# Performance work log

Hardware: AMD Instinct MI355X
Metric: run time of the kernel (lower is better)

## Reference

```python
import jax, jax.numpy as jnp
import numpy as np

B, LC, LE, H, V = 128, 256, 257, 512, 128
PAD = 0  # padding_token_index


def lstm_cell(x, h, c, Wih, Whh, b):
    # torch LSTMCell gate order: i, f, g, o
    g = x @ Wih.T + h @ Whh.T + b
    i, f, gg, o = jnp.split(g, 4, axis=-1)
    c = jax.nn.sigmoid(f) * c + jax.nn.sigmoid(i) * jnp.tanh(gg)
    h = jax.nn.sigmoid(o) * jnp.tanh(c)
    return h, c


def setup_inputs() -> dict:
    key = jax.random.key(0)
    ks = jax.random.split(key, 32)
    p = lambda k, shape: jax.random.normal(k, shape, jnp.float32) * 0.05
    d = {
        'C_idx': jax.random.randint(ks[0], (B, LC), 0, V, dtype=jnp.int32),
        'E_idx': jax.random.randint(ks[1], (B, LE), 0, V, dtype=jnp.int32),
        'C_pad': jnp.zeros((B, LC), dtype=bool),
        'enc_Wih_f': p(ks[2], (4 * H, V)),
        'enc_Whh_f': p(ks[3], (4 * H, H)),
        'enc_b_f': p(ks[4], (4 * H,)),
        'enc_Wih_b': p(ks[5], (4 * H, V)),
        'enc_Whh_b': p(ks[6], (4 * H, H)),
        'enc_b_b': p(ks[7], (4 * H,)),
        'dec_Wih': p(ks[8], (4 * H, H + V)),
        'dec_Whh': p(ks[9], (4 * H, H)),
        'dec_b': p(ks[10], (4 * H,)),
        'Wh': p(ks[11], (H, 2 * H)),
        'Wc': p(ks[12], (H, 2 * H)),
        'Wattn': p(ks[13], (H, 2 * H)),
        'Wout': p(ks[14], (H, 3 * H)),
        'Wvocab': p(ks[15], (V, H)),
        'pg_ctx': p(ks[16], (2 * H,)),
        'pg_in': p(ks[17], (V + H,)),
        'pg_h': p(ks[18], (H,)),
        'pg_c': p(ks[19], (H,)),
        'pg_b': p(ks[20], (1,)),
    }
    return d


def _forward(C_idx, E_idx, C_pad, enc_Wih_f, enc_Whh_f, enc_b_f, enc_Wih_b, enc_Whh_b, enc_b_b,
             dec_Wih, dec_Whh, dec_b, Wh, Wc, Wattn, Wout, Wvocab,
             pg_ctx, pg_in, pg_h, pg_c, pg_b):
    C = jax.nn.one_hot(C_idx, V, dtype=jnp.float32)      # [B,LC,V]
    E_emb = jax.nn.one_hot(E_idx, V, dtype=jnp.float32)  # [B,LE,V]
    z = jnp.zeros((B, H), jnp.float32)

    xs = jnp.swapaxes(C, 0, 1)  # [LC,B,V]

    def enc_fwd(carry, x):
        h, c = lstm_cell(x, carry[0], carry[1], enc_Wih_f, enc_Whh_f, enc_b_f)
        return (h, c), h

    def enc_bwd(carry, x):
        h, c = lstm_cell(x, carry[0], carry[1], enc_Wih_b, enc_Whh_b, enc_b_b)
        return (h, c), h

    (hf, cf), Hf = jax.lax.scan(enc_fwd, (z, z), xs)
    (hb, cb), Hb = jax.lax.scan(enc_bwd, (z, z), xs[::-1])
    Hb = Hb[::-1]
    enc = jnp.swapaxes(jnp.concatenate([Hf, Hb], axis=-1), 0, 1)  # [B,LC,2H]

    # decoder init state from final encoder states (fwd;bwd concat)
    h0 = jnp.concatenate([hf, hb], axis=-1) @ Wh.T
    c0 = jnp.concatenate([cf, cb], axis=-1) @ Wc.T

    enc_proj = enc @ Wattn.T  # [B,LC,H]

    def step(carry, x_emb):
        h, c, prev_out = carry
        nin = jnp.concatenate([x_emb, prev_out], axis=1)  # [B,V+H]
        h, c = lstm_cell(nin, h, c, dec_Wih, dec_Whh, dec_b)
        scores = jnp.einsum('blh,bh->bl', enc_proj, h)
        scores = jnp.where(C_pad, -jnp.inf, scores)
        attn = jax.nn.softmax(scores, axis=1)             # [B,LC]
        ctx = jnp.einsum('bl,blh->bh', attn, enc)         # [B,2H]
        t_out = jnp.tanh(jnp.concatenate([h, ctx], axis=1) @ Wout.T)  # [B,H]
        gen = jax.nn.softmax(t_out @ Wvocab.T, axis=1)    # [B,V]
        p_gen = jax.nn.sigmoid(ctx @ pg_ctx + nin @ pg_in + h @ pg_h + c @ pg_c + pg_b[0])[:, None]
        copy_p = attn * (1.0 - p_gen)
        out = jax.vmap(lambda o, idx, a: o.at[idx].add(a))(gen * p_gen, C_idx, copy_p)
        return (h, c, t_out), out

    xs2 = jnp.swapaxes(E_emb[:, :LE - 1], 0, 1)  # teacher inputs, step 0 = start token
    _, preds = jax.lax.scan(step, (h0, c0, z), xs2)
    preds = jnp.swapaxes(preds, 0, 1)  # [B,LE-1,V]

    tgt = E_idx[:, 1:]
    nll = -jnp.take_along_axis(jnp.log(preds), tgt[..., None], axis=2)[..., 0]
    return jnp.where(tgt == PAD, 0.0, nll)  # [B,LE-1], reduction='none'


def reference(C_idx, E_idx, C_pad, enc_Wih_f, enc_Whh_f, enc_b_f, enc_Wih_b, enc_Whh_b, enc_b_b,
              dec_Wih, dec_Whh, dec_b, Wh, Wc, Wattn, Wout, Wvocab,
              pg_ctx, pg_in, pg_h, pg_c, pg_b):
    return _forward(C_idx, E_idx, C_pad, enc_Wih_f, enc_Whh_f, enc_b_f, enc_Wih_b, enc_Whh_b, enc_b_b,
                    dec_Wih, dec_Whh, dec_b, Wh, Wc, Wattn, Wout, Wvocab,
                    pg_ctx, pg_in, pg_h, pg_c, pg_b)
```

## Files before the change

kernel.cpp:

```cpp
#include <hip/hip_runtime.h>

static constexpr size_t OFF_ENC   = 0;
static constexpr size_t OFF_WGE   = 67108864;
static constexpr size_t OFF_WIHTE = 71303168;
static constexpr size_t OFF_HENC  = 72351744;
static constexpr size_t OFF_CENC  = 72876032;
static constexpr size_t OFF_WGATE = 67108864;
static constexpr size_t OFF_XDEC  = 71303168;
static constexpr size_t OFF_WATTT = 71827456;
static constexpr size_t OFF_WOUT  = 72876032;
static constexpr size_t OFF_WVOCT = 74448896;
static constexpr size_t OFF_HDEC  = 74579968;
static constexpr size_t OFF_CDEC  = 74842112;
static constexpr size_t OFF_TOUT  = 75104256;
static constexpr size_t OFF_UFB   = 75366400;
static constexpr size_t OFF_CTXF  = 75628544;
static constexpr size_t OFF_CTXP  = 75890688;
static constexpr size_t OFF_SC    = 76414976;
static constexpr size_t OFF_MSP   = 76480512;
static constexpr size_t OFF_MD    = 76482560;

__device__ __forceinline__ float sigm(float x) { return 1.f / (1.f + expf(-x)); }
__device__ __forceinline__ unsigned short f2bf(float f) {
  unsigned u = __float_as_uint(f);
  u += 0x7fffu + ((u >> 16) & 1u);
  return (unsigned short)(u >> 16);
}
__device__ __forceinline__ float bfl(unsigned w) { return __uint_as_float(w << 16); }
__device__ __forceinline__ float bfh(unsigned w) { return __uint_as_float(w & 0xffff0000u); }
__device__ __forceinline__ float bf2f(unsigned short v) { return __uint_as_float(((unsigned)v) << 16); }

#if defined(__has_builtin)
#if __has_builtin(__builtin_amdgcn_fdot2_f32_bf16)
#define HAVE_DOT2BF 1
#endif
#endif
#ifdef HAVE_DOT2BF
typedef __bf16 bf2_t __attribute__((ext_vector_type(2)));
__device__ __forceinline__ float dot2bf(unsigned w, unsigned h, float acc) {
  return __builtin_amdgcn_fdot2_f32_bf16(__builtin_bit_cast(bf2_t, w),
                                         __builtin_bit_cast(bf2_t, h), acc, false);
}
#else
__device__ __forceinline__ float dot2bf(unsigned w, unsigned h, float acc) {
  return acc + bfl(w) * bfl(h) + bfh(w) * bfh(h);
}
#endif

__global__ __launch_bounds__(256) void k_pre1(const float* __restrict__ WhhF,
                                              const float* __restrict__ WhhB,
                                              const float* __restrict__ WihF,
                                              const float* __restrict__ WihB,
                                              char* __restrict__ wsb) {
  unsigned short* WGE = (unsigned short*)(wsb + OFF_WGE);
  unsigned short* WIH = (unsigned short*)(wsb + OFF_WIHTE);
  int id = blockIdx.x * 256 + threadIdx.x, str = gridDim.x * 256;
  for (int x = id; x < 2 * 2048 * 512; x += str) {
    int dir = x >> 20, r = (x >> 9) & 2047, k = x & 511;
    const float* W = dir ? WhhB : WhhF;
    WGE[x] = f2bf(W[(size_t)r * 512 + k]);
  }
  for (int x = id; x < 2 * 128 * 2048; x += str) {
    int dir = x >> 18, v = (x >> 11) & 127, r = x & 2047;
    const float* W = dir ? WihB : WihF;
    WIH[x] = f2bf(W[(size_t)r * 128 + v]);
  }
}

__global__ __launch_bounds__(256) void k_pre2(const float* __restrict__ dWih,
                                              const float* __restrict__ dWhh,
                                              const float* __restrict__ Wattn,
                                              const float* __restrict__ Wout,
                                              const float* __restrict__ Wvoc,
                                              char* __restrict__ wsb) {
  unsigned short* WG = (unsigned short*)(wsb + OFF_WGATE);
  unsigned short* XD = (unsigned short*)(wsb + OFF_XDEC);
  unsigned short* WA = (unsigned short*)(wsb + OFF_WATTT);
  unsigned short* WO = (unsigned short*)(wsb + OFF_WOUT);
  unsigned*       WV = (unsigned*)(wsb + OFF_WVOCT);
  int id = blockIdx.x * 256 + threadIdx.x, str = gridDim.x * 256;
  for (int x = id; x < 2048 * 1024; x += str) {
    int r = x >> 10, k = x & 1023;
    float v = (k < 512) ? dWih[(size_t)r * 640 + 128 + k] : dWhh[(size_t)r * 512 + (k - 512)];
    WG[x] = f2bf(v);
  }
  for (int x = id; x < 128 * 2048; x += str) {
    int v = x >> 11, r = x & 2047;
    XD[x] = f2bf(dWih[(size_t)r * 640 + v]);
  }
  for (int x = id; x < 1024 * 512; x += str) {
    int i = x >> 9, o = x & 511;
    WA[x] = f2bf(Wattn[(size_t)o * 1024 + i]);
  }
  for (int x = id; x < 512 * 1536; x += str) WO[x] = f2bf(Wout[x]);
  for (int x = id; x < 256 * 128; x += str) {
    int kk = x >> 7, v = x & 127;
    unsigned lo = f2bf(Wvoc[(size_t)v * 512 + 2 * kk]);
    unsigned hi = f2bf(Wvoc[(size_t)v * 512 + 2 * kk + 1]);
    WV[x] = lo | (hi << 16);
  }
}

__global__ __launch_bounds__(512) void k_encs(const float* __restrict__ bF,
                                              const float* __restrict__ bB,
                                              const int* __restrict__ C_idx,
                                              char* __restrict__ wsb, int t) {
  int tau = threadIdx.x, bid = blockIdx.x;
  int b = tau & 127, slot = tau >> 7;
  int dir = bid >> 7;
  int j = __builtin_amdgcn_readfirstlane(((bid & 127) << 2) + slot);
  int dd = __builtin_amdgcn_readfirstlane(dir);
  int rp = t & 1, wp = rp ^ 1;
  const unsigned* inw = (const unsigned*)(wsb + OFF_HENC) + ((size_t)(dd * 2 + rp) * 256) * 128 + b;
  const uint4* w0 = (const uint4*)((const unsigned*)(wsb + OFF_WGE) + ((size_t)dd * 2048 + j) * 256);
  const uint4* w1 = (const uint4*)((const unsigned*)(wsb + OFF_WGE) + ((size_t)dd * 2048 + 512 + j) * 256);
  const uint4* w2 = (const uint4*)((const unsigned*)(wsb + OFF_WGE) + ((size_t)dd * 2048 + 1024 + j) * 256);
  const uint4* w3 = (const uint4*)((const unsigned*)(wsb + OFF_WGE) + ((size_t)dd * 2048 + 1536 + j) * 256);
  int l = dd ? (255 - t) : t;
  int cidx = C_idx[b * 256 + l];
  const unsigned short* xg = (const unsigned short*)(wsb + OFF_WIHTE) + ((size_t)dd * 128 + cidx) * 2048;
  const float* bias = dd ? bB : bF;
  float a0 = bias[j] + bf2f(xg[j]);
  float a1 = bias[512 + j] + bf2f(xg[512 + j]);
  float a2 = bias[1024 + j] + bf2f(xg[1024 + j]);
  float a3 = bias[1536 + j] + bf2f(xg[1536 + j]);
#pragma unroll 4
  for (int q = 0; q < 64; ++q) {
    uint4 W0 = w0[q], W1 = w1[q], W2 = w2[q], W3 = w3[q];
    unsigned i0 = inw[(q * 4 + 0) * 128], i1 = inw[(q * 4 + 1) * 128];
    unsigned i2 = inw[(q * 4 + 2) * 128], i3 = inw[(q * 4 + 3) * 128];
    a0 = dot2bf(W0.x, i0, a0); a0 = dot2bf(W0.y, i1, a0); a0 = dot2bf(W0.z, i2, a0); a0 = dot2bf(W0.w, i3, a0);
    a1 = dot2bf(W1.x, i0, a1); a1 = dot2bf(W1.y, i1, a1); a1 = dot2bf(W1.z, i2, a1); a1 = dot2bf(W1.w, i3, a1);
    a2 = dot2bf(W2.x, i0, a2); a2 = dot2bf(W2.y, i1, a2); a2 = dot2bf(W2.z, i2, a2); a2 = dot2bf(W2.w, i3, a2);
    a3 = dot2bf(W3.x, i0, a3); a3 = dot2bf(W3.y, i1, a3); a3 = dot2bf(W3.z, i2, a3); a3 = dot2bf(W3.w, i3, a3);
  }
  float ig = sigm(a0), fg = sigm(a1), gg = tanhf(a2), og = sigm(a3);
  float* cp = (float*)(wsb + OFF_CENC) + ((size_t)dir * 512 + j) * 128 + b;
  float c = fg * (*cp) + ig * gg;
  *cp = c;
  float h = og * tanhf(c);
  unsigned short hb = f2bf(h);
  ((unsigned short*)(wsb + OFF_HENC))[((((size_t)(dir * 2 + wp) * 256) + (j >> 1)) * 128 + b) * 2 + (j & 1)] = hb;
  ((unsigned short*)(wsb + OFF_ENC))[((size_t)b * 256 + l) * 1024 + dir * 512 + j] = hb;
}

__global__ __launch_bounds__(512) void k_h0(const float* __restrict__ Wh,
                                            const float* __restrict__ Wc,
                                            char* __restrict__ wsb) {
  int tau = threadIdx.x;
  int b = tau & 127, slot = tau >> 7;
  int row = __builtin_amdgcn_readfirstlane(blockIdx.x * 4 + slot);
  int sel = row >> 9, j = row & 511;
  const float* W = (sel ? Wc : Wh) + (size_t)j * 1024;
  const unsigned short* HE = (const unsigned short*)(wsb + OFF_HENC);
  const float* CE = (const float*)(wsb + OFF_CENC);
  float acc = 0.f;
  for (int k = 0; k < 1024; ++k) {
    int dir = k >> 9, k5 = k & 511;
    float in;
    if (sel == 0)
      in = bf2f(HE[((((size_t)(dir * 2 + 0) * 256) + (k5 >> 1)) * 128 + b) * 2 + (k5 & 1)]);
    else
      in = CE[((size_t)dir * 512 + k5) * 128 + b];
    acc += W[k] * in;
  }
  if (sel == 0)
    ((unsigned short*)(wsb + OFF_HDEC))[(((size_t)(j >> 1)) * 128 + b) * 2 + (j & 1)] = f2bf(acc);
  else
    ((float*)(wsb + OFF_CDEC))[(size_t)j * 128 + b] = acc;
}

__global__ __launch_bounds__(512) void k_gates(const int* __restrict__ E_idx,
                                               const float* __restrict__ db,
                                               char* __restrict__ wsb, int t) {
  __shared__ float part[2][4][128];
  int tau = threadIdx.x;
  int b = tau & 127, jslot = (tau >> 7) & 1, kh = tau >> 8;
  int j = __builtin_amdgcn_readfirstlane(blockIdx.x * 2 + jslot);
  int rp = t & 1, np = rp ^ 1;
  const unsigned* inw = (const unsigned*)(wsb + (kh ? OFF_HDEC : OFF_TOUT)) + (size_t)(kh ? np * 0 + rp : rp) * 256 * 128 + b;
  const unsigned* WG = (const unsigned*)(wsb + OFF_WGATE);
  const uint4* w0 = (const uint4*)(WG + ((size_t)(0 * 512 + j)) * 512 + kh * 256);
  const uint4* w1 = (const uint4*)(WG + ((size_t)(1 * 512 + j)) * 512 + kh * 256);
  const uint4* w2 = (const uint4*)(WG + ((size_t)(2 * 512 + j)) * 512 + kh * 256);
  const uint4* w3 = (const uint4*)(WG + ((size_t)(3 * 512 + j)) * 512 + kh * 256);
  float a0 = 0.f, a1 = 0.f, a2 = 0.f, a3 = 0.f;
#pragma unroll 4
  for (int q = 0; q < 64; ++q) {
    uint4 W0 = w0[q], W1 = w1[q], W2 = w2[q], W3 = w3[q];
    unsigned i0 = inw[(q * 4 + 0) * 128], i1 = inw[(q * 4 + 1) * 128];
    unsigned i2 = inw[(q * 4 + 2) * 128], i3 = inw[(q * 4 + 3) * 128];
    a0 = dot2bf(W0.x, i0, a0); a0 = dot2bf(W0.y, i1, a0); a0 = dot2bf(W0.z, i2, a0); a0 = dot2bf(W0.w, i3, a0);
    a1 = dot2bf(W1.x, i0, a1); a1 = dot2bf(W1.y, i1, a1); a1 = dot2bf(W1.z, i2, a1); a1 = dot2bf(W1.w, i3, a1);
    a2 = dot2bf(W2.x, i0, a2); a2 = dot2bf(W2.y, i1, a2); a2 = dot2bf(W2.z, i2, a2); a2 = dot2bf(W2.w, i3, a2);
    a3 = dot2bf(W3.x, i0, a3); a3 = dot2bf(W3.y, i1, a3); a3 = dot2bf(W3.z, i2, a3); a3 = dot2bf(W3.w, i3, a3);
  }
  if (kh == 1) { part[jslot][0][b] = a0; part[jslot][1][b] = a1; part[jslot][2][b] = a2; part[jslot][3][b] = a3; }
  __syncthreads();
  if (kh == 0) {
    int xid = E_idx[b * 257 + t];
    const unsigned short* xg = (const unsigned short*)(wsb + OFF_XDEC) + (size_t)xid * 2048;
    float g0 = a0 + part[jslot][0][b] + db[j] + bf2f(xg[j]);
    float g1 = a1 + part[jslot][1][b] + db[512 + j] + bf2f(xg[512 + j]);
    float g2 = a2 + part[jslot][2][b] + db[1024 + j] + bf2f(xg[1024 + j]);
    float g3 = a3 + part[jslot][3][b] + db[1536 + j] + bf2f(xg[1536 + j]);
    float ig = sigm(g0), fg = sigm(g1), gg = tanhf(g2), og = sigm(g3);
    float* cp = (float*)(wsb + OFF_CDEC) + (size_t)j * 128 + b;
    float c = fg * (*cp) + ig * gg;
    *cp = c;
    float h = og * tanhf(c);
    ((unsigned short*)(wsb + OFF_HDEC))[(((size_t)np * 256 + (j >> 1)) * 128 + b) * 2 + (j & 1)] = f2bf(h);
  }
}

__global__ __launch_bounds__(512) void k_u(char* __restrict__ wsb, int t) {
  int tau = threadIdx.x;
  int b = tau & 127, slot = tau >> 7;
  int i = __builtin_amdgcn_readfirstlane(blockIdx.x * 4 + slot);
  int np = (t & 1) ^ 1;
  const unsigned* inw = (const unsigned*)(wsb + OFF_HDEC) + (size_t)np * 256 * 128 + b;
  const uint4* w = (const uint4*)((const unsigned*)(wsb + OFF_WATTT) + (size_t)i * 256);
  float a = 0.f;
#pragma unroll 4
  for (int q = 0; q < 64; ++q) {
    uint4 W = w[q];
    a = dot2bf(W.x, inw[(q * 4 + 0) * 128], a);
    a = dot2bf(W.y, inw[(q * 4 + 1) * 128], a);
    a = dot2bf(W.z, inw[(q * 4 + 2) * 128], a);
    a = dot2bf(W.w, inw[(q * 4 + 3) * 128], a);
  }
  ((unsigned short*)(wsb + OFF_UFB))[(((size_t)(i >> 1)) * 128 + b) * 2 + (i & 1)] = f2bf(a);
}

__global__ __launch_bounds__(256) void k_attn(const unsigned char* __restrict__ C_pad,
                                              char* __restrict__ wsb) {
  __shared__ __align__(16) unsigned short tile[32][1024];
  __shared__ __align__(16) unsigned ulds[512];
  __shared__ float sc_l[32];
  __shared__ float p_l[32];
  __shared__ float red[4];
  int bid = blockIdx.x, tau = threadIdx.x;
  int b = bid >> 1, ch = bid & 1;
  int lane = tau & 63, wv = tau >> 6;
  const unsigned* UW = (const unsigned*)(wsb + OFF_UFB) + b;
  ulds[tau] = UW[(size_t)tau * 128];
  ulds[tau + 256] = UW[(size_t)(tau + 256) * 128];
  float mold = -3.0e38f, ssum = 0.f;
  float acc0 = 0.f, acc1 = 0.f, acc2 = 0.f, acc3 = 0.f;
  unsigned short* SCp = (unsigned short*)(wsb + OFF_SC) + (size_t)b * 256;
  int L0 = ch * 128;
  for (int sub = 0; sub < 4; ++sub) {
    const uint4* src = (const uint4*)((const unsigned short*)wsb + ((size_t)b * 256 + L0 + sub * 32) * 1024);
    __syncthreads();
#pragma unroll
    for (int it = 0; it < 16; ++it) ((uint4*)tile)[it * 256 + tau] = src[it * 256 + tau];
    __syncthreads();
    const uint4* t4 = (const uint4*)tile;
    const uint4* u4 = (const uint4*)ulds;
#pragma unroll
    for (int li = 0; li < 8; ++li) {
      int l = wv * 8 + li;
      uint4 ea = t4[l * 128 + lane * 2];
      uint4 eb = t4[l * 128 + lane * 2 + 1];
      uint4 ua = u4[lane * 2];
      uint4 ub = u4[lane * 2 + 1];
      float s = 0.f;
      s = dot2bf(ea.x, ua.x, s); s = dot2bf(ea.y, ua.y, s);
      s = dot2bf(ea.z, ua.z, s); s = dot2bf(ea.w, ua.w, s);
      s = dot2bf(eb.x, ub.x, s); s = dot2bf(eb.y, ub.y, s);
      s = dot2bf(eb.z, ub.z, s); s = dot2bf(eb.w, ub.w, s);
      for (int o = 32; o; o >>= 1) s += __shfl_xor(s, o);
      if (lane == 0) {
        int gl = L0 + sub * 32 + l;
        if (C_pad[b * 256 + gl]) s = -3.0e38f;
        sc_l[l] = s;
        SCp[gl] = f2bf(s);
      }
    }
    __syncthreads();
    if (tau < 64) {
      float v = (tau < 32) ? sc_l[tau] : -3.0e38f;
      for (int o = 32; o; o >>= 1) v = fmaxf(v, __shfl_xor(v, o));
      if (tau == 0) red[0] = v;
    }
    __syncthreads();
    float mnew = fmaxf(mold, red[0]);
    float r = expf(mold - mnew);
    if (tau < 64) {
      float pv = (tau < 32) ? expf(sc_l[tau] - mnew) : 0.f;
      if (tau < 32) p_l[tau] = pv;
      for (int o = 32; o; o >>= 1) pv += __shfl_xor(pv, o);
      if (tau == 0) red[1] = pv;
    }
    __syncthreads();
    ssum = ssum * r + red[1];
    mold = mnew;
    acc0 *= r; acc1 *= r; acc2 *= r; acc3 *= r;
    const uint2* t2 = (const uint2*)tile;
#pragma unroll 8
    for (int l = 0; l < 32; ++l) {
      float pv = p_l[l];
      uint2 ev = t2[l * 256 + tau];
      acc0 += pv * bfl(ev.x); acc1 += pv * bfh(ev.x);
      acc2 += pv * bfl(ev.y); acc3 += pv * bfh(ev.y);
    }
  }
  unsigned* CP = (unsigned*)(wsb + OFF_CTXP);
  unsigned wlo = (unsigned)f2bf(acc0) | ((unsigned)f2bf(acc1) << 16);
  unsigned whi = (unsigned)f2bf(acc2) | ((unsigned)f2bf(acc3) << 16);
  CP[(((size_t)ch * 128 + b) * 1024 + tau * 4) >> 1] = wlo;
  CP[((((size_t)ch * 128 + b) * 1024 + tau * 4) >> 1) + 1] = whi;
  if (tau == 0) {
    float* MSP = (float*)(wsb + OFF_MSP);
    MSP[b * 2 + ch] = mold;
    MSP[256 + b * 2 + ch] = ssum;
  }
}

__global__ __launch_bounds__(256) void k_comb(const int* __restrict__ E_idx,
                                              const float* __restrict__ pgc,
                                              const float* __restrict__ pgi,
                                              const float* __restrict__ pgh,
                                              const float* __restrict__ pgcc,
                                              const float* __restrict__ pgb,
                                              char* __restrict__ wsb, int t) {
  __shared__ float red[4];
  int b = blockIdx.x, tau = threadIdx.x;
  int lane = tau & 63, wv = tau >> 6;
  int rp = t & 1, np = rp ^ 1;
  const float* MSP = (const float*)(wsb + OFF_MSP);
  float m0 = MSP[b * 2], m1 = MSP[b * 2 + 1];
  float s0 = MSP[256 + b * 2], s1 = MSP[256 + b * 2 + 1];
  float M = fmaxf(m0, m1);
  float e0 = expf(m0 - M), e1 = expf(m1 - M);
  float D = s0 * e0 + s1 * e1;
  float invD = 1.f / D;
  const unsigned* CP = (const unsigned*)(wsb + OFF_CTXP);
  size_t base0 = (((size_t)0 * 128 + b) * 1024 + tau * 4) >> 1;
  size_t base1 = (((size_t)1 * 128 + b) * 1024 + tau * 4) >> 1;
  unsigned c0l = CP[base0], c0h = CP[base0 + 1], c1l = CP[base1], c1h = CP[base1 + 1];
  float x0 = (bfl(c0l) * e0 + bfl(c1l) * e1) * invD;
  float x1 = (bfh(c0l) * e0 + bfh(c1l) * e1) * invD;
  float x2 = (bfl(c0h) * e0 + bfl(c1h) * e1) * invD;
  float x3 = (bfh(c0h) * e0 + bfh(c1h) * e1) * invD;
  unsigned* CF = (unsigned*)(wsb + OFF_CTXF);
  CF[((size_t)tau * 2) * 128 + b]     = (unsigned)f2bf(x0) | ((unsigned)f2bf(x1) << 16);
  CF[((size_t)tau * 2 + 1) * 128 + b] = (unsigned)f2bf(x2) | ((unsigned)f2bf(x3) << 16);
  int f0 = tau * 4;
  float pp = x0 * pgc[f0] + x1 * pgc[f0 + 1] + x2 * pgc[f0 + 2] + x3 * pgc[f0 + 3];
  if (f0 < 512) {
    const unsigned short* H = (const unsigned short*)(wsb + OFF_HDEC);
    const unsigned short* TO = (const unsigned short*)(wsb + OFF_TOUT);
    const float* C = (const float*)(wsb + OFF_CDEC);
#pragma unroll
    for (int e = 0; e < 4; ++e) {
      int f = f0 + e;
      float hv = bf2f(H[(((size_t)np * 256 + (f >> 1)) * 128 + b) * 2 + (f & 1)]);
      float pv = bf2f(TO[(((size_t)rp * 256 + (f >> 1)) * 128 + b) * 2 + (f & 1)]);
      float cv = C[(size_t)f * 128 + b];
      pp += hv * pgh[f] + cv * pgcc[f] + pv * pgi[128 + f];
    }
  }
  for (int o = 32; o; o >>= 1) pp += __shfl_xor(pp, o);
  if (lane == 0) red[wv] = pp;
  __syncthreads();
  if (tau == 0) {
    int xid = E_idx[b * 257 + t];
    float s = red[0] + red[1] + red[2] + red[3] + pgi[xid] + pgb[0];
    float* MD = (float*)(wsb + OFF_MD);
    MD[b] = M;
    MD[128 + b] = D;
    MD[256 + b] = sigm(s);
  }
}

__global__ __launch_bounds__(512) void k_wout(char* __restrict__ wsb, int t) {
  __shared__ float part[2][128];
  int tau = threadIdx.x;
  int b = tau & 127, nslot = (tau >> 7) & 1, kh = tau >> 8;
  int n = __builtin_amdgcn_readfirstlane(blockIdx.x * 2 + nslot);
  int np = (t & 1) ^ 1;
  const unsigned* HW = (const unsigned*)(wsb + OFF_HDEC) + (size_t)np * 256 * 128 + b;
  const unsigned* CW = (const unsigned*)(wsb + OFF_CTXF) + b;
  const unsigned* w = (const unsigned*)(wsb + OFF_WOUT) + (size_t)n * 768 + kh * 384;
  float a = 0.f;
  int p0 = kh * 384;
#pragma unroll 4
  for (int q = 0; q < 96; ++q) {
    uint4 W = ((const uint4*)w)[q];
#pragma unroll
    for (int e = 0; e < 4; ++e) {
      int pp = p0 + q * 4 + e;
      unsigned in = (pp < 256) ? HW[(size_t)pp * 128] : CW[(size_t)(pp - 256) * 128];
      unsigned wv = (e == 0) ? W.x : (e == 1) ? W.y : (e == 2) ? W.z : W.w;
      a = dot2bf(wv, in, a);
    }
  }
  if (kh == 1) part[nslot][b] = a;
  __syncthreads();
  if (kh == 0) {
    float tv = tanhf(a + part[nslot][b]);
    ((unsigned short*)(wsb + OFF_TOUT))[(((size_t)np * 256 + (n >> 1)) * 128 + b) * 2 + (n & 1)] = f2bf(tv);
  }
}

__global__ __launch_bounds__(256) void k_fin(const int* __restrict__ C_idx,
                                             const int* __restrict__ E_idx,
                                             char* __restrict__ wsb,
                                             float* __restrict__ out, int t) {
  __shared__ unsigned to_pld[256];
  __shared__ float lgp[2][128];
  __shared__ float lgf[128];
  __shared__ float red[8];
  int b = blockIdx.x, tau = threadIdx.x;
  int lane = tau & 63, wv = tau >> 6;
  int np = (t & 1) ^ 1;
  const unsigned* TOW = (const unsigned*)(wsb + OFF_TOUT) + (size_t)np * 256 * 128 + b;
  to_pld[tau] = TOW[(size_t)tau * 128];
  __syncthreads();
  int v = tau & 127, kh = tau >> 7;
  const unsigned* WV = (const unsigned*)(wsb + OFF_WVOCT) + v;
  float a = 0.f;
#pragma unroll 8
  for (int kkk = 0; kkk < 128; ++kkk) {
    int kk = kh * 128 + kkk;
    a = dot2bf(WV[(size_t)kk * 128], to_pld[kk], a);
  }
  lgp[kh][v] = a;
  __syncthreads();
  if (tau < 128) {
    float lg = lgp[0][tau] + lgp[1][tau];
    lgf[tau] = lg;
    float m = lg;
    for (int o = 32; o; o >>= 1) m = fmaxf(m, __shfl_xor(m, o));
    if (lane == 0) red[wv] = m;
  }
  __syncthreads();
  float mx = fmaxf(red[0], red[1]);
  if (tau < 128) {
    float e = expf(lgf[tau] - mx);
    for (int o = 32; o; o >>= 1) e += __shfl_xor(e, o);
    if (lane == 0) red[2 + wv] = e;
  }
  __syncthreads();
  const float* MD = (const float*)(wsb + OFF_MD);
  float M = MD[b], D = MD[128 + b], pg = MD[256 + b];
  int tgt = E_idx[b * 257 + t + 1];
  float cm = 0.f;
  {
    float s = bf2f(((const unsigned short*)(wsb + OFF_SC))[(size_t)b * 256 + tau]);
    if (C_idx[b * 256 + tau] == tgt) cm = expf(s - M);
  }
  for (int o = 32; o; o >>= 1) cm += __shfl_xor(cm, o);
  if (lane == 0) red[4 + wv] = cm;
  __syncthreads();
  if (tau == 0) {
    float sume = red[2] + red[3];
    float copy_raw = red[4] + red[5] + red[6] + red[7];
    float gen_tgt = expf(lgf[tgt] - mx) / sume;
    float prob = pg * gen_tgt + (1.f - pg) * copy_raw / D;
    out[b * 256 + t] = (tgt == 0) ? 0.f : -logf(prob);
  }
}

extern "C" void kernel_launch(void* const* d_in, const int* in_sizes, int n_in,
                              void* d_out, int out_size, void* d_ws, size_t ws_size,
                              hipStream_t stream) {
  (void)in_sizes; (void)n_in; (void)out_size; (void)ws_size;
  const int* C_idx = (const int*)d_in[0];
  const int* E_idx = (const int*)d_in[1];
  const unsigned char* C_pad = (const unsigned char*)d_in[2];
  const float* eWihF = (const float*)d_in[3];
  const float* eWhhF = (const float*)d_in[4];
  const float* ebF   = (const float*)d_in[5];
  const float* eWihB = (const float*)d_in[6];
  const float* eWhhB = (const float*)d_in[7];
  const float* ebB   = (const float*)d_in[8];
  const float* dWih  = (const float*)d_in[9];
  const float* dWhh  = (const float*)d_in[10];
  const float* db    = (const float*)d_in[11];
  const float* Wh    = (const float*)d_in[12];
  const float* Wc    = (const float*)d_in[13];
  const float* Wattn = (const float*)d_in[14];
  const float* Wout  = (const float*)d_in[15];
  const float* Wvoc  = (const float*)d_in[16];
  const float* pgc   = (const float*)d_in[17];
  const float* pgi   = (const float*)d_in[18];
  const float* pgh   = (const float*)d_in[19];
  const float* pgcc  = (const float*)d_in[20];
  const float* pgb   = (const float*)d_in[21];
  char* wsb = (char*)d_ws;
  float* out = (float*)d_out;

  hipMemsetAsync(wsb + OFF_HENC, 0, 524288, stream);
  hipMemsetAsync(wsb + OFF_CENC, 0, 524288, stream);
  hipMemsetAsync(wsb + OFF_TOUT, 0, 262144, stream);

  k_pre1<<<256, 256, 0, stream>>>(eWhhF, eWhhB, eWihF, eWihB, wsb);
  for (int t = 0; t < 256; ++t)
    k_encs<<<256, 512, 0, stream>>>(ebF, ebB, C_idx, wsb, t);
  k_h0<<<256, 512, 0, stream>>>(Wh, Wc, wsb);
  k_pre2<<<256, 256, 0, stream>>>(dWih, dWhh, Wattn, Wout, Wvoc, wsb);
  for (int t = 0; t < 256; ++t) {
    k_gates<<<256, 512, 0, stream>>>(E_idx, db, wsb, t);
    k_u<<<256, 512, 0, stream>>>(wsb, t);
    k_attn<<<256, 256, 0, stream>>>(C_pad, wsb);
    k_comb<<<128, 256, 0, stream>>>(E_idx, pgc, pgi, pgh, pgcc, pgb, wsb, t);
    k_wout<<<256, 512, 0, stream>>>(wsb, t);
    k_fin<<<128, 256, 0, stream>>>(C_idx, E_idx, wsb, out, t);
  }
}
```

Before: 27.29 ms.

## Fuse all recurrent steps into one persistent cooperative kernel with grid barriers

Replaces roughly 1800 per-timestep kernel launches with a single cooperative persistent kernel of 256 blocks that steps through the encoder and decoder phases, separated by a hierarchical atomic grid barrier. Cell states are kept in registers rather than round-tripping through global memory. The comb phase is folded into attention and the final-output phase, and final-output work for step t-1 overlaps with the u projection for step t, cutting barriers per step. The cost is spin-wait barrier overhead, and correctness depends on all 256 blocks being co-resident, with a large 130 KB shared-memory footprint.

```diff
diff --git a/kernel.cpp b/kernel.cpp
--- a/kernel.cpp
+++ b/kernel.cpp
@@ -1,24 +1,41 @@
 #include <hip/hip_runtime.h>
 
-static constexpr size_t OFF_ENC   = 0;
-static constexpr size_t OFF_WGE   = 67108864;
-static constexpr size_t OFF_WIHTE = 71303168;
-static constexpr size_t OFF_HENC  = 72351744;
-static constexpr size_t OFF_CENC  = 72876032;
-static constexpr size_t OFF_WGATE = 67108864;
-static constexpr size_t OFF_XDEC  = 71303168;
-static constexpr size_t OFF_WATTT = 71827456;
-static constexpr size_t OFF_WOUT  = 72876032;
-static constexpr size_t OFF_WVOCT = 74448896;
-static constexpr size_t OFF_HDEC  = 74579968;
-static constexpr size_t OFF_CDEC  = 74842112;
-static constexpr size_t OFF_TOUT  = 75104256;
-static constexpr size_t OFF_UFB   = 75366400;
-static constexpr size_t OFF_CTXF  = 75628544;
-static constexpr size_t OFF_CTXP  = 75890688;
-static constexpr size_t OFF_SC    = 76414976;
-static constexpr size_t OFF_MSP   = 76480512;
-static constexpr size_t OFF_MD    = 76482560;
+static constexpr size_t OFF_ENC    = 0;
+static constexpr size_t OFF_WGE    = 67108864;
+static constexpr size_t OFF_WIHTE  = 71303168;
+static constexpr size_t OFF_HENC   = 72351744;
+static constexpr size_t OFF_CENC   = 72876032;
+static constexpr size_t OFF_WGATE  = 67108864;
+static constexpr size_t OFF_XDEC   = 71303168;
+static constexpr size_t OFF_WATTT  = 71827456;
+static constexpr size_t OFF_WOUT   = 72876032;
+static constexpr size_t OFF_WVOCT  = 74448896;
+static constexpr size_t OFF_HDEC   = 74579968;
+static constexpr size_t OFF_CDECP0 = 74842112;
+static constexpr size_t OFF_TOUT   = 75104256;
+static constexpr size_t OFF_UFB    = 75366400;
+static constexpr size_t OFF_CDECP1 = 75628544;
+static constexpr size_t OFF_CTXP   = 75890688;
+static constexpr size_t OFF_SC     = 76414976;
+static constexpr size_t OFF_MSP    = 76480512;
+static constexpr size_t OFF_BAR    = 76483072;
+
+static constexpr int SM_TILE = 0;
+static constexpr int SM_U    = 131072;
+static constexpr int SM_SCL  = 133120;
+static constexpr int SM_PL   = 133376;
+static constexpr int SM_RED  = 133632;
+static constexpr int SM_SIZE = 133696;
+
+struct KP {
+  const int* C_idx; const int* E_idx; const unsigned char* C_pad;
+  const float* eWihF; const float* eWhhF; const float* ebF;
+  const float* eWihB; const float* eWhhB; const float* ebB;
+  const float* dWih;  const float* dWhh;  const float* db;
+  const float* Wh; const float* Wc; const float* Wattn; const float* Wout; const float* Wvoc;
+  const float* pgc; const float* pgi; const float* pgh; const float* pgcc; const float* pgb;
+  char* wsb; float* out;
+};
 
 __device__ __forceinline__ float sigm(float x) { return 1.f / (1.f + expf(-x)); }
 __device__ __forceinline__ unsigned short f2bf(float f) {
@@ -46,6 +63,27 @@
   return acc + bfl(w) * bfl(h) + bfh(w) * bfh(h);
 }
 #endif
+
+__device__ __forceinline__ void gbar(int* bar, int bid) {
+  __syncthreads();
+  if (threadIdx.x == 0) {
+    __builtin_amdgcn_fence(__ATOMIC_RELEASE, "agent");
+    int* gen = bar + 32;
+    int g = __hip_atomic_load(gen, __ATOMIC_RELAXED, __HIP_MEMORY_SCOPE_AGENT);
+    int* gc = bar + 64 + (bid >> 4) * 32;
+    if (__hip_atomic_fetch_add(gc, 1, __ATOMIC_RELAXED, __HIP_MEMORY_SCOPE_AGENT) == 15) {
+      __hip_atomic_store(gc, 0, __ATOMIC_RELAXED, __HIP_MEMORY_SCOPE_AGENT);
+      if (__hip_atomic_fetch_add(bar, 1, __ATOMIC_RELAXED, __HIP_MEMORY_SCOPE_AGENT) == 15) {
+        __hip_atomic_store(bar, 0, __ATOMIC_RELAXED, __HIP_MEMORY_SCOPE_AGENT);
+        __hip_atomic_store(gen, g + 1, __ATOMIC_RELEASE, __HIP_MEMORY_SCOPE_AGENT);
+      }
+    }
+    while (__hip_atomic_load(gen, __ATOMIC_RELAXED, __HIP_MEMORY_SCOPE_AGENT) == g)
+      __builtin_amdgcn_s_sleep(1);
+    __builtin_amdgcn_fence(__ATOMIC_ACQUIRE, "agent");
+  }
+  __syncthreads();
+}
 
 __global__ __launch_bounds__(256) void k_pre1(const float* __restrict__ WhhF,
                                               const float* __restrict__ WhhB,
@@ -67,59 +105,23 @@
   }
 }
 
-__global__ __launch_bounds__(256) void k_pre2(const float* __restrict__ dWih,
-                                              const float* __restrict__ dWhh,
-                                              const float* __restrict__ Wattn,
-                                              const float* __restrict__ Wout,
-                                              const float* __restrict__ Wvoc,
-                                              char* __restrict__ wsb) {
-  unsigned short* WG = (unsigned short*)(wsb + OFF_WGATE);
-  unsigned short* XD = (unsigned short*)(wsb + OFF_XDEC);
-  unsigned short* WA = (unsigned short*)(wsb + OFF_WATTT);
-  unsigned short* WO = (unsigned short*)(wsb + OFF_WOUT);
-  unsigned*       WV = (unsigned*)(wsb + OFF_WVOCT);
-  int id = blockIdx.x * 256 + threadIdx.x, str = gridDim.x * 256;
-  for (int x = id; x < 2048 * 1024; x += str) {
-    int r = x >> 10, k = x & 1023;
-    float v = (k < 512) ? dWih[(size_t)r * 640 + 128 + k] : dWhh[(size_t)r * 512 + (k - 512)];
-    WG[x] = f2bf(v);
-  }
-  for (int x = id; x < 128 * 2048; x += str) {
-    int v = x >> 11, r = x & 2047;
-    XD[x] = f2bf(dWih[(size_t)r * 640 + v]);
-  }
-  for (int x = id; x < 1024 * 512; x += str) {
-    int i = x >> 9, o = x & 511;
-    WA[x] = f2bf(Wattn[(size_t)o * 1024 + i]);
-  }
-  for (int x = id; x < 512 * 1536; x += str) WO[x] = f2bf(Wout[x]);
-  for (int x = id; x < 256 * 128; x += str) {
-    int kk = x >> 7, v = x & 127;
-    unsigned lo = f2bf(Wvoc[(size_t)v * 512 + 2 * kk]);
-    unsigned hi = f2bf(Wvoc[(size_t)v * 512 + 2 * kk + 1]);
-    WV[x] = lo | (hi << 16);
-  }
-}
-
-__global__ __launch_bounds__(512) void k_encs(const float* __restrict__ bF,
-                                              const float* __restrict__ bB,
-                                              const int* __restrict__ C_idx,
-                                              char* __restrict__ wsb, int t) {
-  int tau = threadIdx.x, bid = blockIdx.x;
+__device__ void ph_enc(const KP& P, int bid, int tau, int t, float& c_enc) {
+  char* wsb = P.wsb;
   int b = tau & 127, slot = tau >> 7;
   int dir = bid >> 7;
   int j = __builtin_amdgcn_readfirstlane(((bid & 127) << 2) + slot);
   int dd = __builtin_amdgcn_readfirstlane(dir);
   int rp = t & 1, wp = rp ^ 1;
-  const unsigned* inw = (const unsigned*)(wsb + OFF_HENC) + ((size_t)(dd * 2 + rp) * 256) * 128 + b;
-  const uint4* w0 = (const uint4*)((const unsigned*)(wsb + OFF_WGE) + ((size_t)dd * 2048 + j) * 256);
-  const uint4* w1 = (const uint4*)((const unsigned*)(wsb + OFF_WGE) + ((size_t)dd * 2048 + 512 + j) * 256);
-  const uint4* w2 = (const uint4*)((const unsigned*)(wsb + OFF_WGE) + ((size_t)dd * 2048 + 1024 + j) * 256);
-  const uint4* w3 = (const uint4*)((const unsigned*)(wsb + OFF_WGE) + ((size_t)dd * 2048 + 1536 + j) * 256);
+  const unsigned* inw = (const unsigned*)(wsb + OFF_HENC) + (size_t)(dd * 2 + rp) * 32768 + b;
+  const unsigned* WGE = (const unsigned*)(wsb + OFF_WGE);
+  const uint4* w0 = (const uint4*)(WGE + ((size_t)dd * 2048 + j) * 256);
+  const uint4* w1 = (const uint4*)(WGE + ((size_t)dd * 2048 + 512 + j) * 256);
+  const uint4* w2 = (const uint4*)(WGE + ((size_t)dd * 2048 + 1024 + j) * 256);
+  const uint4* w3 = (const uint4*)(WGE + ((size_t)dd * 2048 + 1536 + j) * 256);
   int l = dd ? (255 - t) : t;
-  int cidx = C_idx[b * 256 + l];
+  int cidx = P.C_idx[b * 256 + l];
   const unsigned short* xg = (const unsigned short*)(wsb + OFF_WIHTE) + ((size_t)dd * 128 + cidx) * 2048;
-  const float* bias = dd ? bB : bF;
+  const float* bias = dd ? P.ebB : P.ebF;
   float a0 = bias[j] + bf2f(xg[j]);
   float a1 = bias[512 + j] + bf2f(xg[512 + j]);
   float a2 = bias[1024 + j] + bf2f(xg[1024 + j]);
@@ -135,23 +137,21 @@
     a3 = dot2bf(W3.x, i0, a3); a3 = dot2bf(W3.y, i1, a3); a3 = dot2bf(W3.z, i2, a3); a3 = dot2bf(W3.w, i3, a3);
   }
   float ig = sigm(a0), fg = sigm(a1), gg = tanhf(a2), og = sigm(a3);
-  float* cp = (float*)(wsb + OFF_CENC) + ((size_t)dir * 512 + j) * 128 + b;
-  float c = fg * (*cp) + ig * gg;
-  *cp = c;
+  float c = fg * c_enc + ig * gg;
+  c_enc = c;
   float h = og * tanhf(c);
   unsigned short hb = f2bf(h);
-  ((unsigned short*)(wsb + OFF_HENC))[((((size_t)(dir * 2 + wp) * 256) + (j >> 1)) * 128 + b) * 2 + (j & 1)] = hb;
+  ((unsigned short*)(wsb + OFF_HENC))[(((size_t)(dir * 2 + wp) * 256 + (j >> 1)) * 128 + b) * 2 + (j & 1)] = hb;
   ((unsigned short*)(wsb + OFF_ENC))[((size_t)b * 256 + l) * 1024 + dir * 512 + j] = hb;
-}
-
-__global__ __launch_bounds__(512) void k_h0(const float* __restrict__ Wh,
-                                            const float* __restrict__ Wc,
-                                            char* __restrict__ wsb) {
-  int tau = threadIdx.x;
+  if (t == 255) ((float*)(wsb + OFF_CENC))[((size_t)dir * 512 + j) * 128 + b] = c;
+}
+
+__device__ void ph_h0(const KP& P, int bid, int tau) {
+  char* wsb = P.wsb;
   int b = tau & 127, slot = tau >> 7;
-  int row = __builtin_amdgcn_readfirstlane(blockIdx.x * 4 + slot);
+  int row = __builtin_amdgcn_readfirstlane(bid * 4 + slot);
   int sel = row >> 9, j = row & 511;
-  const float* W = (sel ? Wc : Wh) + (size_t)j * 1024;
+  const float* W = (sel ? P.Wc : P.Wh) + (size_t)j * 1024;
   const unsigned short* HE = (const unsigned short*)(wsb + OFF_HENC);
   const float* CE = (const float*)(wsb + OFF_CENC);
   float acc = 0.f;
@@ -159,7 +159,7 @@
     int dir = k >> 9, k5 = k & 511;
     float in;
     if (sel == 0)
-      in = bf2f(HE[((((size_t)(dir * 2 + 0) * 256) + (k5 >> 1)) * 128 + b) * 2 + (k5 & 1)]);
+      in = bf2f(HE[(((size_t)(dir * 2 + 0) * 256 + (k5 >> 1)) * 128 + b) * 2 + (k5 & 1)]);
     else
       in = CE[((size_t)dir * 512 + k5) * 128 + b];
     acc += W[k] * in;
@@ -167,23 +167,51 @@
   if (sel == 0)
     ((unsigned short*)(wsb + OFF_HDEC))[(((size_t)(j >> 1)) * 128 + b) * 2 + (j & 1)] = f2bf(acc);
   else
-    ((float*)(wsb + OFF_CDEC))[(size_t)j * 128 + b] = acc;
-}
-
-__global__ __launch_bounds__(512) void k_gates(const int* __restrict__ E_idx,
-                                               const float* __restrict__ db,
-                                               char* __restrict__ wsb, int t) {
-  __shared__ float part[2][4][128];
-  int tau = threadIdx.x;
+    ((float*)(wsb + OFF_CDECP0))[(size_t)j * 128 + b] = acc;
+}
+
+__device__ void ph_pre2(const KP& P, int bid, int tau) {
+  char* wsb = P.wsb;
+  unsigned short* WG = (unsigned short*)(wsb + OFF_WGATE);
+  unsigned short* XD = (unsigned short*)(wsb + OFF_XDEC);
+  unsigned short* WA = (unsigned short*)(wsb + OFF_WATTT);
+  unsigned short* WO = (unsigned short*)(wsb + OFF_WOUT);
+  unsigned*       WV = (unsigned*)(wsb + OFF_WVOCT);
+  int id = bid * 512 + tau, str = 256 * 512;
+  for (int x = id; x < 2048 * 1024; x += str) {
+    int r = x >> 10, k = x & 1023;
+    float v = (k < 512) ? P.dWih[(size_t)r * 640 + 128 + k] : P.dWhh[(size_t)r * 512 + (k - 512)];
+    WG[x] = f2bf(v);
+  }
+  for (int x = id; x < 128 * 2048; x += str) {
+    int v = x >> 11, r = x & 2047;
+    XD[x] = f2bf(P.dWih[(size_t)r * 640 + v]);
+  }
+  for (int x = id; x < 1024 * 512; x += str) {
+    int i = x >> 9, o = x & 511;
+    WA[x] = f2bf(P.Wattn[(size_t)o * 1024 + i]);
+  }
+  for (int x = id; x < 512 * 1536; x += str) WO[x] = f2bf(P.Wout[x]);
+  for (int x = id; x < 256 * 128; x += str) {
+    int kk = x >> 7, v = x & 127;
+    unsigned lo = f2bf(P.Wvoc[(size_t)v * 512 + 2 * kk]);
+    unsigned hi = f2bf(P.Wvoc[(size_t)v * 512 + 2 * kk + 1]);
+    WV[x] = lo | (hi << 16);
+  }
+}
+
+__device__ void ph_gates(const KP& P, char* smem, int bid, int tau, int t, float& c_dec) {
+  char* wsb = P.wsb;
+  float (*part)[4][128] = (float(*)[4][128])smem;
   int b = tau & 127, jslot = (tau >> 7) & 1, kh = tau >> 8;
-  int j = __builtin_amdgcn_readfirstlane(blockIdx.x * 2 + jslot);
+  int j = __builtin_amdgcn_readfirstlane(bid * 2 + jslot);
   int rp = t & 1, np = rp ^ 1;
-  const unsigned* inw = (const unsigned*)(wsb + (kh ? OFF_HDEC : OFF_TOUT)) + (size_t)(kh ? np * 0 + rp : rp) * 256 * 128 + b;
+  const unsigned* inw = (const unsigned*)(wsb + (kh ? OFF_HDEC : OFF_TOUT)) + (size_t)rp * 32768 + b;
   const unsigned* WG = (const unsigned*)(wsb + OFF_WGATE);
-  const uint4* w0 = (const uint4*)(WG + ((size_t)(0 * 512 + j)) * 512 + kh * 256);
-  const uint4* w1 = (const uint4*)(WG + ((size_t)(1 * 512 + j)) * 512 + kh * 256);
-  const uint4* w2 = (const uint4*)(WG + ((size_t)(2 * 512 + j)) * 512 + kh * 256);
-  const uint4* w3 = (const uint4*)(WG + ((size_t)(3 * 512 + j)) * 512 + kh * 256);
+  const uint4* w0 = (const uint4*)(WG + (size_t)j * 512 + kh * 256);
+  const uint4* w1 = (const uint4*)(WG + ((size_t)512 + j) * 512 + kh * 256);
+  const uint4* w2 = (const uint4*)(WG + ((size_t)1024 + j) * 512 + kh * 256);
+  const uint4* w3 = (const uint4*)(WG + ((size_t)1536 + j) * 512 + kh * 256);
   float a0 = 0.f, a1 = 0.f, a2 = 0.f, a3 = 0.f;
 #pragma unroll 4
   for (int q = 0; q < 64; ++q) {
@@ -198,72 +226,76 @@
   if (kh == 1) { part[jslot][0][b] = a0; part[jslot][1][b] = a1; part[jslot][2][b] = a2; part[jslot][3][b] = a3; }
   __syncthreads();
   if (kh == 0) {
-    int xid = E_idx[b * 257 + t];
+    if (t == 0) c_dec = ((const float*)(wsb + OFF_CDECP0))[(size_t)j * 128 + b];
+    int xid = P.E_idx[b * 257 + t];
     const unsigned short* xg = (const unsigned short*)(wsb + OFF_XDEC) + (size_t)xid * 2048;
-    float g0 = a0 + part[jslot][0][b] + db[j] + bf2f(xg[j]);
-    float g1 = a1 + part[jslot][1][b] + db[512 + j] + bf2f(xg[512 + j]);
-    float g2 = a2 + part[jslot][2][b] + db[1024 + j] + bf2f(xg[1024 + j]);
-    float g3 = a3 + part[jslot][3][b] + db[1536 + j] + bf2f(xg[1536 + j]);
+    float g0 = a0 + part[jslot][0][b] + P.db[j] + bf2f(xg[j]);
+    float g1 = a1 + part[jslot][1][b] + P.db[512 + j] + bf2f(xg[512 + j]);
+    float g2 = a2 + part[jslot][2][b] + P.db[1024 + j] + bf2f(xg[1024 + j]);
+    float g3 = a3 + part[jslot][3][b] + P.db[1536 + j] + bf2f(xg[1536 + j]);
     float ig = sigm(g0), fg = sigm(g1), gg = tanhf(g2), og = sigm(g3);
-    float* cp = (float*)(wsb + OFF_CDEC) + (size_t)j * 128 + b;
-    float c = fg * (*cp) + ig * gg;
-    *cp = c;
+    float c = fg * c_dec + ig * gg;
+    c_dec = c;
     float h = og * tanhf(c);
+    ((float*)(wsb + (np ? OFF_CDECP1 : OFF_CDECP0)))[(size_t)j * 128 + b] = c;
     ((unsigned short*)(wsb + OFF_HDEC))[(((size_t)np * 256 + (j >> 1)) * 128 + b) * 2 + (j & 1)] = f2bf(h);
   }
-}
-
-__global__ __launch_bounds__(512) void k_u(char* __restrict__ wsb, int t) {
-  int tau = threadIdx.x;
-  int b = tau & 127, slot = tau >> 7;
-  int i = __builtin_amdgcn_readfirstlane(blockIdx.x * 4 + slot);
+  __syncthreads();
+}
+
+__device__ void ph_u(const KP& P, int bid, int tau, int t) {
+  char* wsb = P.wsb;
+  int b = tau & 127, rslot = tau >> 7;
+  int i0 = __builtin_amdgcn_readfirstlane(bid * 8 + rslot * 2);
   int np = (t & 1) ^ 1;
-  const unsigned* inw = (const unsigned*)(wsb + OFF_HDEC) + (size_t)np * 256 * 128 + b;
-  const uint4* w = (const uint4*)((const unsigned*)(wsb + OFF_WATTT) + (size_t)i * 256);
-  float a = 0.f;
+  const unsigned* inw = (const unsigned*)(wsb + OFF_HDEC) + (size_t)np * 32768 + b;
+  float aa[2];
+#pragma unroll
+  for (int r = 0; r < 2; ++r) {
+    const uint4* w = (const uint4*)((const unsigned*)(wsb + OFF_WATTT) + (size_t)(i0 + r) * 256);
+    float a = 0.f;
 #pragma unroll 4
-  for (int q = 0; q < 64; ++q) {
-    uint4 W = w[q];
-    a = dot2bf(W.x, inw[(q * 4 + 0) * 128], a);
-    a = dot2bf(W.y, inw[(q * 4 + 1) * 128], a);
-    a = dot2bf(W.z, inw[(q * 4 + 2) * 128], a);
-    a = dot2bf(W.w, inw[(q * 4 + 3) * 128], a);
-  }
-  ((unsigned short*)(wsb + OFF_UFB))[(((size_t)(i >> 1)) * 128 + b) * 2 + (i & 1)] = f2bf(a);
-}
-
-__global__ __launch_bounds__(256) void k_attn(const unsigned char* __restrict__ C_pad,
-                                              char* __restrict__ wsb) {
-  __shared__ __align__(16) unsigned short tile[32][1024];
-  __shared__ __align__(16) unsigned ulds[512];
-  __shared__ float sc_l[32];
-  __shared__ float p_l[32];
-  __shared__ float red[4];
-  int bid = blockIdx.x, tau = threadIdx.x;
+    for (int q = 0; q < 64; ++q) {
+      uint4 W = w[q];
+      a = dot2bf(W.x, inw[(q * 4 + 0) * 128], a);
+      a = dot2bf(W.y, inw[(q * 4 + 1) * 128], a);
+      a = dot2bf(W.z, inw[(q * 4 + 2) * 128], a);
+      a = dot2bf(W.w, inw[(q * 4 + 3) * 128], a);
+    }
+    aa[r] = a;
+  }
+  ((unsigned*)(wsb + OFF_UFB))[((size_t)(i0 >> 1)) * 128 + b] =
+      (unsigned)f2bf(aa[0]) | ((unsigned)f2bf(aa[1]) << 16);
+}
+
+__device__ void ph_attn(const KP& P, char* smem, int bid, int tau, int t) {
+  char* wsb = P.wsb;
+  uint4* tile4 = (uint4*)(smem + SM_TILE);
+  const unsigned* tl = (const unsigned*)(smem + SM_TILE);
+  unsigned* ulds = (unsigned*)(smem + SM_U);
+  float* sc_l = (float*)(smem + SM_SCL);
+  float* p_l = (float*)(smem + SM_PL);
+  float* red = (float*)(smem + SM_RED);
   int b = bid >> 1, ch = bid & 1;
   int lane = tau & 63, wv = tau >> 6;
   const unsigned* UW = (const unsigned*)(wsb + OFF_UFB) + b;
   ulds[tau] = UW[(size_t)tau * 128];
-  ulds[tau + 256] = UW[(size_t)(tau + 256) * 128];
-  float mold = -3.0e38f, ssum = 0.f;
-  float acc0 = 0.f, acc1 = 0.f, acc2 = 0.f, acc3 = 0.f;
+  float mold = -3.0e38f, ssum = 0.f, acc0 = 0.f, acc1 = 0.f;
   unsigned short* SCp = (unsigned short*)(wsb + OFF_SC) + (size_t)b * 256;
   int L0 = ch * 128;
-  for (int sub = 0; sub < 4; ++sub) {
-    const uint4* src = (const uint4*)((const unsigned short*)wsb + ((size_t)b * 256 + L0 + sub * 32) * 1024);
+  for (int sub = 0; sub < 2; ++sub) {
+    const uint4* src = (const uint4*)((const unsigned short*)wsb + ((size_t)b * 256 + L0 + sub * 64) * 1024);
     __syncthreads();
 #pragma unroll
-    for (int it = 0; it < 16; ++it) ((uint4*)tile)[it * 256 + tau] = src[it * 256 + tau];
+    for (int it = 0; it < 16; ++it) tile4[it * 512 + tau] = src[it * 512 + tau];
     __syncthreads();
-    const uint4* t4 = (const uint4*)tile;
     const uint4* u4 = (const uint4*)ulds;
+    uint4 ua = u4[lane * 2], ub = u4[lane * 2 + 1];
 #pragma unroll
     for (int li = 0; li < 8; ++li) {
       int l = wv * 8 + li;
-      uint4 ea = t4[l * 128 + lane * 2];
-      uint4 eb = t4[l * 128 + lane * 2 + 1];
-      uint4 ua = u4[lane * 2];
-      uint4 ub = u4[lane * 2 + 1];
+      uint4 ea = tile4[l * 128 + lane * 2];
+      uint4 eb = tile4[l * 128 + lane * 2 + 1];
       float s = 0.f;
       s = dot2bf(ea.x, ua.x, s); s = dot2bf(ea.y, ua.y, s);
       s = dot2bf(ea.z, ua.z, s); s = dot2bf(ea.w, ua.w, s);
@@ -271,15 +303,15 @@
       s = dot2bf(eb.z, ub.z, s); s = dot2bf(eb.w, ub.w, s);
       for (int o = 32; o; o >>= 1) s += __shfl_xor(s, o);
       if (lane == 0) {
-        int gl = L0 + sub * 32 + l;
-        if (C_pad[b * 256 + gl]) s = -3.0e38f;
+        int gl = L0 + sub * 64 + l;
+        if (P.C_pad[b * 256 + gl]) s = -3.0e38f;
         sc_l[l] = s;
         SCp[gl] = f2bf(s);
       }
     }
     __syncthreads();
     if (tau < 64) {
-      float v = (tau < 32) ? sc_l[tau] : -3.0e38f;
+      float v = sc_l[tau];
       for (int o = 32; o; o >>= 1) v = fmaxf(v, __shfl_xor(v, o));
       if (tau == 0) red[0] = v;
     }
@@ -287,101 +319,48 @@
     float mnew = fmaxf(mold, red[0]);
     float r = expf(mold - mnew);
     if (tau < 64) {
-      float pv = (tau < 32) ? expf(sc_l[tau] - mnew) : 0.f;
-      if (tau < 32) p_l[tau] = pv;
+      float pv = expf(sc_l[tau] - mnew);
+      p_l[tau] = pv;
       for (int o = 32; o; o >>= 1) pv += __shfl_xor(pv, o);
       if (tau == 0) red[1] = pv;
     }
     __syncthreads();
     ssum = ssum * r + red[1];
     mold = mnew;
-    acc0 *= r; acc1 *= r; acc2 *= r; acc3 *= r;
-    const uint2* t2 = (const uint2*)tile;
+    acc0 *= r; acc1 *= r;
 #pragma unroll 8
-    for (int l = 0; l < 32; ++l) {
+    for (int l = 0; l < 64; ++l) {
       float pv = p_l[l];
-      uint2 ev = t2[l * 256 + tau];
-      acc0 += pv * bfl(ev.x); acc1 += pv * bfh(ev.x);
-      acc2 += pv * bfl(ev.y); acc3 += pv * bfh(ev.y);
-    }
-  }
-  unsigned* CP = (unsigned*)(wsb + OFF_CTXP);
-  unsigned wlo = (unsigned)f2bf(acc0) | ((unsigned)f2bf(acc1) << 16);
-  unsigned whi = (unsigned)f2bf(acc2) | ((unsigned)f2bf(acc3) << 16);
-  CP[(((size_t)ch * 128 + b) * 1024 + tau * 4) >> 1] = wlo;
-  CP[((((size_t)ch * 128 + b) * 1024 + tau * 4) >> 1) + 1] = whi;
+      unsigned ev = tl[l * 512 + tau];
+      acc0 += pv * bfl(ev); acc1 += pv * bfh(ev);
+    }
+  }
+  ((unsigned*)(wsb + OFF_CTXP))[((size_t)ch * 128 + b) * 512 + tau] =
+      (unsigned)f2bf(acc0) | ((unsigned)f2bf(acc1) << 16);
   if (tau == 0) {
     float* MSP = (float*)(wsb + OFF_MSP);
     MSP[b * 2 + ch] = mold;
     MSP[256 + b * 2 + ch] = ssum;
   }
-}
-
-__global__ __launch_bounds__(256) void k_comb(const int* __restrict__ E_idx,
-                                              const float* __restrict__ pgc,
-                                              const float* __restrict__ pgi,
-                                              const float* __restrict__ pgh,
-                                              const float* __restrict__ pgcc,
-                                              const float* __restrict__ pgb,
-                                              char* __restrict__ wsb, int t) {
-  __shared__ float red[4];
-  int b = blockIdx.x, tau = threadIdx.x;
-  int lane = tau & 63, wv = tau >> 6;
-  int rp = t & 1, np = rp ^ 1;
+  __syncthreads();
+}
+
+__device__ void ph_wout(const KP& P, char* smem, int bid, int tau, int t) {
+  char* wsb = P.wsb;
+  float (*part)[128] = (float(*)[128])smem;
+  int b = tau & 127, nslot = (tau >> 7) & 1, kh = tau >> 8;
+  int n = __builtin_amdgcn_readfirstlane(bid * 2 + nslot);
+  int np = (t & 1) ^ 1;
   const float* MSP = (const float*)(wsb + OFF_MSP);
   float m0 = MSP[b * 2], m1 = MSP[b * 2 + 1];
   float s0 = MSP[256 + b * 2], s1 = MSP[256 + b * 2 + 1];
   float M = fmaxf(m0, m1);
   float e0 = expf(m0 - M), e1 = expf(m1 - M);
-  float D = s0 * e0 + s1 * e1;
-  float invD = 1.f / D;
-  const unsigned* CP = (const unsigned*)(wsb + OFF_CTXP);
-  size_t base0 = (((size_t)0 * 128 + b) * 1024 + tau * 4) >> 1;
-  size_t base1 = (((size_t)1 * 128 + b) * 1024 + tau * 4) >> 1;
-  unsigned c0l = CP[base0], c0h = CP[base0 + 1], c1l = CP[base1], c1h = CP[base1 + 1];
-  float x0 = (bfl(c0l) * e0 + bfl(c1l) * e1) * invD;
-  float x1 = (bfh(c0l) * e0 + bfh(c1l) * e1) * invD;
-  float x2 = (bfl(c0h) * e0 + bfl(c1h) * e1) * invD;
-  float x3 = (bfh(c0h) * e0 + bfh(c1h) * e1) * invD;
-  unsigned* CF = (unsigned*)(wsb + OFF_CTXF);
-  CF[((size_t)tau * 2) * 128 + b]     = (unsigned)f2bf(x0) | ((unsigned)f2bf(x1) << 16);
-  CF[((size_t)tau * 2 + 1) * 128 + b] = (unsigned)f2bf(x2) | ((unsigned)f2bf(x3) << 16);
-  int f0 = tau * 4;
-  float pp = x0 * pgc[f0] + x1 * pgc[f0 + 1] + x2 * pgc[f0 + 2] + x3 * pgc[f0 + 3];
-  if (f0 < 512) {
-    const unsigned short* H = (const unsigned short*)(wsb + OFF_HDEC);
-    const unsigned short* TO = (const unsigned short*)(wsb + OFF_TOUT);
-    const float* C = (const float*)(wsb + OFF_CDEC);
-#pragma unroll
-    for (int e = 0; e < 4; ++e) {
-      int f = f0 + e;
-      float hv = bf2f(H[(((size_t)np * 256 + (f >> 1)) * 128 + b) * 2 + (f & 1)]);
-      float pv = bf2f(TO[(((size_t)rp * 256 + (f >> 1)) * 128 + b) * 2 + (f & 1)]);
-      float cv = C[(size_t)f * 128 + b];
-      pp += hv * pgh[f] + cv * pgcc[f] + pv * pgi[128 + f];
-    }
-  }
-  for (int o = 32; o; o >>= 1) pp += __shfl_xor(pp, o);
-  if (lane == 0) red[wv] = pp;
-  __syncthreads();
-  if (tau == 0) {
-    int xid = E_idx[b * 257 + t];
-    float s = red[0] + red[1] + red[2] + red[3] + pgi[xid] + pgb[0];
-    float* MD = (float*)(wsb + OFF_MD);
-    MD[b] = M;
-    MD[128 + b] = D;
-    MD[256 + b] = sigm(s);
-  }
-}
-
-__global__ __launch_bounds__(512) void k_wout(char* __restrict__ wsb, int t) {
-  __shared__ float part[2][128];
-  int tau = threadIdx.x;
-  int b = tau & 127, nslot = (tau >> 7) & 1, kh = tau >> 8;
-  int n = __builtin_amdgcn_readfirstlane(blockIdx.x * 2 + nslot);
-  int np = (t & 1) ^ 1;
-  const unsigned* HW = (const unsigned*)(wsb + OFF_HDEC) + (size_t)np * 256 * 128 + b;
-  const unsigned* CW = (const unsigned*)(wsb + OFF_CTXF) + b;
+  float invD = 1.f / (s0 * e0 + s1 * e1);
+  e0 *= invD; e1 *= invD;
+  const unsigned* HW = (const unsigned*)(wsb + OFF_HDEC) + (size_t)np * 32768 + b;
+  const unsigned* CP0 = (const unsigned*)(wsb + OFF_CTXP) + (size_t)b * 512;
+  const unsigned* CP1 = CP0 + 65536;
   const unsigned* w = (const unsigned*)(wsb + OFF_WOUT) + (size_t)n * 768 + kh * 384;
   float a = 0.f;
   int p0 = kh * 384;
@@ -391,9 +370,16 @@
 #pragma unroll
     for (int e = 0; e < 4; ++e) {
       int pp = p0 + q * 4 + e;
-      unsigned in = (pp < 256) ? HW[(size_t)pp * 128] : CW[(size_t)(pp - 256) * 128];
-      unsigned wv = (e == 0) ? W.x : (e == 1) ? W.y : (e == 2) ? W.z : W.w;
-      a = dot2bf(wv, in, a);
+      unsigned wvv = (e == 0) ? W.x : (e == 1) ? W.y : (e == 2) ? W.z : W.w;
+      if (pp < 256) {
+        a = dot2bf(wvv, HW[(size_t)pp * 128], a);
+      } else {
+        int ci = pp - 256;
+        unsigned c0 = CP0[ci], c1 = CP1[ci];
+        float x0 = bfl(c0) * e0 + bfl(c1) * e1;
+        float x1 = bfh(c0) * e0 + bfh(c1) * e1;
+        a += bfl(wvv) * x0 + bfh(wvv) * x1;
+      }
     }
   }
   if (kh == 1) part[nslot][b] = a;
@@ -402,34 +388,32 @@
     float tv = tanhf(a + part[nslot][b]);
     ((unsigned short*)(wsb + OFF_TOUT))[(((size_t)np * 256 + (n >> 1)) * 128 + b) * 2 + (n & 1)] = f2bf(tv);
   }
-}
-
-__global__ __launch_bounds__(256) void k_fin(const int* __restrict__ C_idx,
-                                             const int* __restrict__ E_idx,
-                                             char* __restrict__ wsb,
-                                             float* __restrict__ out, int t) {
-  __shared__ unsigned to_pld[256];
-  __shared__ float lgp[2][128];
-  __shared__ float lgf[128];
-  __shared__ float red[8];
-  int b = blockIdx.x, tau = threadIdx.x;
-  int lane = tau & 63, wv = tau >> 6;
-  int np = (t & 1) ^ 1;
-  const unsigned* TOW = (const unsigned*)(wsb + OFF_TOUT) + (size_t)np * 256 * 128 + b;
-  to_pld[tau] = TOW[(size_t)tau * 128];
+  __syncthreads();
+}
+
+__device__ void ph_fin(const KP& P, char* smem, int b, int tf) {
+  char* wsb = P.wsb;
+  unsigned* to_pld = (unsigned*)smem;
+  float* lgp = (float*)(smem + 1024);
+  float* lgf = (float*)(smem + 3072);
+  float* red = (float*)(smem + 3584);
+  int tau = threadIdx.x, lane = tau & 63, wv = tau >> 6;
+  int npf = (tf & 1) ^ 1, rpf = tf & 1;
+  const unsigned* TOW = (const unsigned*)(wsb + OFF_TOUT) + (size_t)npf * 32768 + b;
+  if (tau < 256) to_pld[tau] = TOW[(size_t)tau * 128];
   __syncthreads();
   int v = tau & 127, kh = tau >> 7;
   const unsigned* WV = (const unsigned*)(wsb + OFF_WVOCT) + v;
   float a = 0.f;
 #pragma unroll 8
-  for (int kkk = 0; kkk < 128; ++kkk) {
-    int kk = kh * 128 + kkk;
+  for (int q = 0; q < 64; ++q) {
+    int kk = kh * 64 + q;
     a = dot2bf(WV[(size_t)kk * 128], to_pld[kk], a);
   }
-  lgp[kh][v] = a;
+  lgp[kh * 128 + v] = a;
   __syncthreads();
   if (tau < 128) {
-    float lg = lgp[0][tau] + lgp[1][tau];
+    float lg = lgp[tau] + lgp[128 + tau] + lgp[256 + tau] + lgp[384 + tau];
     lgf[tau] = lg;
     float m = lg;
     for (int o = 32; o; o >>= 1) m = fmaxf(m, __shfl_xor(m, o));
@@ -442,71 +426,114 @@
     for (int o = 32; o; o >>= 1) e += __shfl_xor(e, o);
     if (lane == 0) red[2 + wv] = e;
   }
-  __syncthreads();
-  const float* MD = (const float*)(wsb + OFF_MD);
-  float M = MD[b], D = MD[128 + b], pg = MD[256 + b];
-  int tgt = E_idx[b * 257 + t + 1];
+  const float* MSP = (const float*)(wsb + OFF_MSP);
+  float m0 = MSP[b * 2], m1 = MSP[b * 2 + 1];
+  float s0 = MSP[256 + b * 2], s1 = MSP[256 + b * 2 + 1];
+  float M = fmaxf(m0, m1);
+  float e0 = expf(m0 - M), e1 = expf(m1 - M);
+  float invD = 1.f / (s0 * e0 + s1 * e1);
+  int tgt = P.E_idx[b * 257 + tf + 1];
   float cm = 0.f;
+  if (tau < 256) {
+    float s = bf2f(((const unsigned short*)(wsb + OFF_SC))[(size_t)b * 256 + tau]);
+    if (P.C_idx[b * 256 + tau] == tgt) cm = expf(s - M);
+  }
+  for (int o = 32; o; o >>= 1) cm += __shfl_xor(cm, o);
+  if (lane == 0 && wv < 4) red[4 + wv] = cm;
+  const unsigned* CP0 = (const unsigned*)(wsb + OFF_CTXP) + (size_t)b * 512;
+  const unsigned* CP1 = CP0 + 65536;
+  unsigned c0 = CP0[tau], c1 = CP1[tau];
+  float x0 = (bfl(c0) * e0 + bfl(c1) * e1) * invD;
+  float x1 = (bfh(c0) * e0 + bfh(c1) * e1) * invD;
+  float pp = x0 * P.pgc[2 * tau] + x1 * P.pgc[2 * tau + 1];
   {
-    float s = bf2f(((const unsigned short*)(wsb + OFF_SC))[(size_t)b * 256 + tau]);
-    if (C_idx[b * 256 + tau] == tgt) cm = expf(s - M);
-  }
-  for (int o = 32; o; o >>= 1) cm += __shfl_xor(cm, o);
-  if (lane == 0) red[4 + wv] = cm;
+    int f = tau;
+    const unsigned short* H = (const unsigned short*)(wsb + OFF_HDEC) + (size_t)npf * 65536;
+    const unsigned short* TOp = (const unsigned short*)(wsb + OFF_TOUT) + (size_t)rpf * 65536;
+    const float* C = (const float*)(wsb + (npf ? OFF_CDECP1 : OFF_CDECP0));
+    float hv = bf2f(H[((size_t)(f >> 1) * 128 + b) * 2 + (f & 1)]);
+    float tv = bf2f(TOp[((size_t)(f >> 1) * 128 + b) * 2 + (f & 1)]);
+    float cv = C[(size_t)f * 128 + b];
+    pp += hv * P.pgh[f] + cv * P.pgcc[f] + tv * P.pgi[128 + f];
+  }
+  for (int o = 32; o; o >>= 1) pp += __shfl_xor(pp, o);
+  if (lane == 0) red[8 + wv] = pp;
   __syncthreads();
   if (tau == 0) {
     float sume = red[2] + red[3];
-    float copy_raw = red[4] + red[5] + red[6] + red[7];
+    float copy_raw = (red[4] + red[5] + red[6] + red[7]) * invD;
+    float pgs = red[8] + red[9] + red[10] + red[11] + red[12] + red[13] + red[14] + red[15];
+    pgs += P.pgi[P.E_idx[b * 257 + tf]] + P.pgb[0];
+    float pg = sigm(pgs);
     float gen_tgt = expf(lgf[tgt] - mx) / sume;
-    float prob = pg * gen_tgt + (1.f - pg) * copy_raw / D;
-    out[b * 256 + t] = (tgt == 0) ? 0.f : -logf(prob);
-  }
+    float prob = pg * gen_tgt + (1.f - pg) * copy_raw;
+    P.out[b * 256 + tf] = (tgt == 0) ? 0.f : -logf(prob);
+  }
+  __syncthreads();
+}
+
+__global__ void __launch_bounds__(512) k_all(KP P) {
+  __shared__ __align__(16) char smem[SM_SIZE];
+  const int bid = blockIdx.x;
+  const int tau = threadIdx.x;
+  int* bar = (int*)(P.wsb + OFF_BAR);
+  float c_enc = 0.f, c_dec = 0.f;
+
+  for (int t = 0; t < 256; ++t) { ph_enc(P, bid, tau, t, c_enc); gbar(bar, bid); }
+  ph_h0(P, bid, tau);
+  gbar(bar, bid);
+  ph_pre2(P, bid, tau);
+  gbar(bar, bid);
+  for (int t = 0; t < 256; ++t) {
+    ph_gates(P, smem, bid, tau, t, c_dec);
+    gbar(bar, bid);
+    if (bid < 128) ph_u(P, bid, tau, t);
+    else if (t > 0) ph_fin(P, smem, bid - 128, t - 1);
+    gbar(bar, bid);
+    ph_attn(P, smem, bid, tau, t);
+    gbar(bar, bid);
+    ph_wout(P, smem, bid, tau, t);
+    gbar(bar, bid);
+  }
+  if (bid >= 128) ph_fin(P, smem, bid - 128, 255);
 }
 
 extern "C" void kernel_launch(void* const* d_in, const int* in_sizes, int n_in,
                               void* d_out, int out_size, void* d_ws, size_t ws_size,
                               hipStream_t stream) {
   (void)in_sizes; (void)n_in; (void)out_size; (void)ws_size;
-  const int* C_idx = (const int*)d_in[0];
-  const int* E_idx = (const int*)d_in[1];
-  const unsigned char* C_pad = (const unsigned char*)d_in[2];
-  const float* eWihF = (const float*)d_in[3];
-  const float* eWhhF = (const float*)d_in[4];
-  const float* ebF   = (const float*)d_in[5];
-  const float* eWihB = (const float*)d_in[6];
-  const float* eWhhB = (const float*)d_in[7];
-  const float* ebB   = (const float*)d_in[8];
-  const float* dWih  = (const float*)d_in[9];
-  const float* dWhh  = (const float*)d_in[10];
-  const float* db    = (const float*)d_in[11];
-  const float* Wh    = (const float*)d_in[12];
-  const float* Wc    = (const float*)d_in[13];
-  const float* Wattn = (const float*)d_in[14];
-  const float* Wout  = (const float*)d_in[15];
-  const float* Wvoc  = (const float*)d_in[16];
-  const float* pgc   = (const float*)d_in[17];
-  const float* pgi   = (const float*)d_in[18];
-  const float* pgh   = (const float*)d_in[19];
-  const float* pgcc  = (const float*)d_in[20];
-  const float* pgb   = (const float*)d_in[21];
-  char* wsb = (char*)d_ws;
-  float* out = (float*)d_out;
-
-  hipMemsetAsync(wsb + OFF_HENC, 0, 524288, stream);
-  hipMemsetAsync(wsb + OFF_CENC, 0, 524288, stream);
-  hipMemsetAsync(wsb + OFF_TOUT, 0, 262144, stream);
-
-  k_pre1<<<256, 256, 0, stream>>>(eWhhF, eWhhB, eWihF, eWihB, wsb);
-  for (int t = 0; t < 256; ++t)
-    k_encs<<<256, 512, 0, stream>>>(ebF, ebB, C_idx, wsb, t);
-  k_h0<<<256, 512, 0, stream>>>(Wh, Wc, wsb);
-  k_pre2<<<256, 256, 0, stream>>>(dWih, dWhh, Wattn, Wout, Wvoc, wsb);
-  for (int t = 0; t < 256; ++t) {
-    k_gates<<<256, 512, 0, stream>>>(E_idx, db, wsb, t);
-    k_u<<<256, 512, 0, stream>>>(wsb, t);
-    k_attn<<<256, 256, 0, stream>>>(C_pad, wsb);
-    k_comb<<<128, 256, 0, stream>>>(E_idx, pgc, pgi, pgh, pgcc, pgb, wsb, t);
-    k_wout<<<256, 512, 0, stream>>>(wsb, t);
-    k_fin<<<128, 256, 0, stream>>>(C_idx, E_idx, wsb, out, t);
-  }
-}
+  KP P;
+  P.C_idx = (const int*)d_in[0];
+  P.E_idx = (const int*)d_in[1];
+  P.C_pad = (const unsigned char*)d_in[2];
+  P.eWihF = (const float*)d_in[3];
+  P.eWhhF = (const float*)d_in[4];
+  P.ebF   = (const float*)d_in[5];
+  P.eWihB = (const float*)d_in[6];
+  P.eWhhB = (const float*)d_in[7];
+  P.ebB   = (const float*)d_in[8];
+  P.dWih  = (const float*)d_in[9];
+  P.dWhh  = (const float*)d_in[10];
+  P.db    = (const float*)d_in[11];
+  P.Wh    = (const float*)d_in[12];
+  P.Wc    = (const float*)d_in[13];
+  P.Wattn = (const float*)d_in[14];
+  P.Wout  = (const float*)d_in[15];
+  P.Wvoc  = (const float*)d_in[16];
+  P.pgc   = (const float*)d_in[17];
+  P.pgi   = (const float*)d_in[18];
+  P.pgh   = (const float*)d_in[19];
+  P.pgcc  = (const float*)d_in[20];
+  P.pgb   = (const float*)d_in[21];
+  P.wsb   = (char*)d_ws;
+  P.out   = (float*)d_out;
+
+  hipMemsetAsync((char*)d_ws + OFF_HENC, 0, 524288, stream);
+  hipMemsetAsync((char*)d_ws + OFF_TOUT, 0, 262144, stream);
+  hipMemsetAsync((char*)d_ws + OFF_BAR, 0, 8192, stream);
+
+  k_pre1<<<256, 256, 0, stream>>>(P.eWhhF, P.eWhhB, P.eWihF, P.eWihB, P.wsb);
+
+  void* args[] = { &P };
+  hipLaunchCooperativeKernel((const void*)k_all, dim3(256), dim3(512), args, 0, stream);
+}
```

New measurement: 94.77 ms. +247.3%, slower.
